# Performance work log

Measured on AMD Instinct MI355X. Metric: run time of the kernel, lower is better.

Reference implementation:

```python
import jax, jax.numpy as jnp
import numpy as np

B, S, E, H = 2, 2048, 2048, 16
D = E // H          # head_dim = 128
RD = 128            # rotary_emb_dim (== head_dim here)
BASE = 10000.0


def setup_inputs() -> dict:
    key = jax.random.key(0)
    k1, k2, k3, k4, k5 = jax.random.split(key, 5)
    scale = 0.02
    return {
        "x": jax.random.normal(k1, (B, S, E), dtype=jnp.float32),
        "wqkv_w": jax.random.normal(k2, (3 * E, E), dtype=jnp.float32) * scale,
        "wqkv_b": jax.random.normal(k3, (3 * E,), dtype=jnp.float32) * scale,
        "out_w": jax.random.normal(k4, (E, E), dtype=jnp.float32) * scale,
        "out_b": jax.random.normal(k5, (E,), dtype=jnp.float32) * scale,
    }


def _rope_cos_sin(seqlen, dtype):
    inv_freq = 1.0 / (BASE ** (jnp.arange(0, RD, 2, dtype=jnp.float32) / RD))
    t = jnp.arange(seqlen, dtype=jnp.float32)
    freqs = jnp.outer(t, inv_freq)          # (S, RD//2)
    return jnp.cos(freqs).astype(dtype), jnp.sin(freqs).astype(dtype)


def _apply_rotary(v, cos, sin):
    # v: (B, S, H, D); rotate first RD dims (here RD == D)
    v_rot, v_pass = v[..., :RD], v[..., RD:]
    v1, v2 = jnp.split(v_rot, 2, axis=-1)    # each (B, S, H, RD//2)
    c = cos[None, :, None, :]
    s = sin[None, :, None, :]
    rot = jnp.concatenate([v1 * c - v2 * s, v1 * s + v2 * c], axis=-1)
    return jnp.concatenate([rot, v_pass], axis=-1)


def reference(x, wqkv_w, wqkv_b, out_w, out_b):
    b, s, e = x.shape
    # column-parallel QKV projection (world size 1)
    qkv = jnp.einsum("bse,fe->bsf", x, wqkv_w) + wqkv_b     # (B, S, 3E)
    qkv = qkv.reshape(b, s, 3, H, D)
    cos, sin = _rope_cos_sin(s, x.dtype)
    q = _apply_rotary(qkv[:, :, 0], cos, sin)               # (B, S, H, D)
    k = _apply_rotary(qkv[:, :, 1], cos, sin)
    v = qkv[:, :, 2]
    # causal self-attention, softmax_scale = 1/sqrt(head_dim)
    scale = 1.0 / jnp.sqrt(jnp.asarray(D, dtype=x.dtype))
    scores = jnp.einsum("bshd,bthd->bhst", q, k) * scale    # (B, H, S, S)
    causal_mask = jnp.tril(jnp.ones((s, s), dtype=bool))
    scores = jnp.where(causal_mask[None, None], scores, jnp.finfo(x.dtype).min)
    probs = jax.nn.softmax(scores, axis=-1)
    ctx = jnp.einsum("bhst,bthd->bshd", probs, v)           # (B, S, H, D)
    # row-parallel output projection
    out = jnp.einsum("bse,fe->bsf", ctx.reshape(b, s, e), out_w) + out_b
    return out
```

## Files before the change

kernel.cpp:

```cpp
#include <hip/hip_runtime.h>
#include <cstdint>
#include <cstddef>

#define Bd 2
#define Sd 2048
#define Ed 2048
#define Hd 16
#define Dd 128
#define N3E 6144
#define ATT_SCALE 0.08838834764831845f

typedef short bf16x8 __attribute__((ext_vector_type(8)));
typedef float f32x4 __attribute__((ext_vector_type(4)));
typedef float f32x16 __attribute__((ext_vector_type(16)));

__device__ __forceinline__ float bf2f(unsigned short u) {
    union { unsigned int u; float f; } c;
    c.u = ((unsigned int)u) << 16;
    return c.f;
}
__device__ __forceinline__ unsigned short f2bf(float f) {
    union { float f; unsigned int u; } c;
    c.f = f;
    unsigned int x = c.u;
    x += 0x7FFFu + ((x >> 16) & 1u);
    return (unsigned short)(x >> 16);
}

__device__ __forceinline__ void gl2lds16(const void* g, void* l) {
    __builtin_amdgcn_global_load_lds(
        (const __attribute__((address_space(1))) void*)g,
        (__attribute__((address_space(3))) void*)l, 16, 0, 0);
}

__global__ void cvt_all(const float* __restrict__ x,
                        const float* __restrict__ w1,
                        const float* __restrict__ w2,
                        unsigned short* __restrict__ ox,
                        unsigned short* __restrict__ o1,
                        unsigned short* __restrict__ o2) {
    int i = (blockIdx.x * 256 + threadIdx.x) * 4;
    const float* s;
    unsigned short* d;
    int off;
    if (i < 8388608) { s = x; d = ox; off = i; }
    else if (i < 20971520) { s = w1; d = o1; off = i - 8388608; }
    else { s = w2; d = o2; off = i - 20971520; }
    const float4 v = *(const float4*)(s + off);
    d[off + 0] = f2bf(v.x);
    d[off + 1] = f2bf(v.y);
    d[off + 2] = f2bf(v.z);
    d[off + 3] = f2bf(v.w);
}

template <int MODE>
__global__ void gemm_bt(const unsigned short* __restrict__ A,
                        const unsigned short* __restrict__ Bm,
                        const float* __restrict__ bias,
                        void* __restrict__ o0, void* __restrict__ o1,
                        void* __restrict__ o2, int Ndim, int K) {
    __shared__ __align__(16) unsigned short U[16640];
    unsigned short* As = U;
    unsigned short* Bs = U + 8192;

    const int tid = threadIdx.x;
    const int lane = tid & 63;
    const int wave = tid >> 6;
    const int quad = lane >> 4;
    const int l16 = lane & 15;
    const int wr = wave >> 1;
    const int wc = wave & 1;

    const int n0 = blockIdx.x * 128;
    const int m0 = blockIdx.y * 128;

    const unsigned short* Ab = A + (size_t)m0 * K;
    const unsigned short* Bb = Bm + (size_t)n0 * K;

    const f32x4 fzero = {0.f, 0.f, 0.f, 0.f};
    f32x4 acc[4][4];
#pragma unroll
    for (int i = 0; i < 4; i++)
#pragma unroll
        for (int j = 0; j < 4; j++) acc[i][j] = fzero;

    for (int k0 = 0; k0 < K; k0 += 64) {
        __syncthreads();
#pragma unroll
        for (int it = 0; it < 4; ++it) {
            int L = it * 256 + tid;
            int row = L >> 3;
            int cs = L & 7;
            int gc = cs ^ (row & 7);
            gl2lds16(Ab + row * K + k0 + gc * 8, (void*)(As + L * 8));
            gl2lds16(Bb + row * K + k0 + gc * 8, (void*)(Bs + L * 8));
        }
        __syncthreads();
#pragma unroll
        for (int kk = 0; kk < 2; ++kk) {
            bf16x8 af[4], bfr[4];
#pragma unroll
            for (int i = 0; i < 4; i++) {
                int row = wr * 64 + i * 16 + l16;
                int cs = kk * 4 + quad;
                af[i] = *(const bf16x8*)(As + row * 64 + (cs ^ (row & 7)) * 8);
            }
#pragma unroll
            for (int j = 0; j < 4; j++) {
                int row = wc * 64 + j * 16 + l16;
                int cs = kk * 4 + quad;
                bfr[j] = *(const bf16x8*)(Bs + row * 64 + (cs ^ (row & 7)) * 8);
            }
#pragma unroll
            for (int i = 0; i < 4; i++)
#pragma unroll
                for (int j = 0; j < 4; j++)
                    acc[i][j] = __builtin_amdgcn_mfma_f32_16x16x32_bf16(
                        af[i], bfr[j], acc[i][j], 0, 0, 0);
        }
    }

    if (MODE == 0) {
#pragma unroll
        for (int j = 0; j < 4; j++) {
            int col = n0 + wc * 64 + j * 16 + l16;
            float bv = bias[col];
#pragma unroll
            for (int i = 0; i < 4; i++) {
                int rbase = m0 + wr * 64 + i * 16 + quad * 4;
#pragma unroll
                for (int r = 0; r < 4; r++)
                    ((float*)o0)[(size_t)(rbase + r) * Ndim + col] =
                        acc[i][j][r] + bv;
            }
        }
    } else {
        __syncthreads();
#pragma unroll
        for (int j = 0; j < 4; j++) {
            int coll = wc * 64 + j * 16 + l16;
            float bv = bias[n0 + coll];
#pragma unroll
            for (int i = 0; i < 4; i++) {
                int rl = wr * 64 + i * 16 + quad * 4;
#pragma unroll
                for (int r = 0; r < 4; r++)
                    U[(rl + r) * 130 + coll] = f2bf(acc[i][j][r] + bv);
            }
        }
        __syncthreads();

        const int ch = n0 >> 7;
        const int c = ch >> 4;
        const int h = ch & 15;
        const int bb = m0 >> 11;
        const int s0 = m0 & 2047;

        if (c < 2) {
            unsigned short* dstq = (unsigned short*)(c == 0 ? o0 : o1);
            const size_t hb = ((size_t)(bb * Hd + h)) * Sd;
#pragma unroll
            for (int it = 0; it < 16; ++it) {
                int lin = it * 256 + tid;
                int row = lin >> 5, p = lin & 31;
                int s = s0 + row;
                unsigned int lo = *(const unsigned int*)(U + row * 130 + 2 * p);
                unsigned int hi =
                    *(const unsigned int*)(U + row * 130 + 64 + 2 * p);
                float v1a = bf2f((unsigned short)lo), v1b = bf2f(lo >> 16);
                float v2a = bf2f((unsigned short)hi), v2b = bf2f(hi >> 16);
                float fa = (float)s * __expf(-(float)(2 * p) *
                                             (9.210340371976184f / 64.0f));
                float fb = (float)s * __expf(-(float)(2 * p + 1) *
                                             (9.210340371976184f / 64.0f));
                float sna, csa, snb, csb;
                __sincosf(fa, &sna, &csa);
                __sincosf(fb, &snb, &csb);
                ushort2 r1, r2;
                r1.x = f2bf(v1a * csa - v2a * sna);
                r1.y = f2bf(v1b * csb - v2b * snb);
                r2.x = f2bf(v1a * sna + v2a * csa);
                r2.y = f2bf(v1b * snb + v2b * csb);
                unsigned short* dst = dstq + (hb + s) * Dd;
                *(ushort2*)(dst + 2 * p) = r1;
                *(ushort2*)(dst + 64 + 2 * p) = r2;
            }
        } else {
            unsigned short* dstv = (unsigned short*)o2;
            const size_t hb = ((size_t)(bb * Hd + h)) * Dd;
#pragma unroll
            for (int it = 0; it < 16; ++it) {
                int lin = it * 256 + tid;
                int d = lin >> 5, sc = lin & 31;
                int s4 = sc * 4;
                ushort4 pk;
                pk.x = U[(s4 + 0) * 130 + d];
                pk.y = U[(s4 + 1) * 130 + d];
                pk.z = U[(s4 + 2) * 130 + d];
                pk.w = U[(s4 + 3) * 130 + d];
                *(ushort4*)(dstv + (hb + d) * Sd + s0 + s4) = pk;
            }
        }
    }
}

__global__ __launch_bounds__(256, 2) void flash_attn(
    const unsigned short* __restrict__ q, const unsigned short* __restrict__ k,
    const unsigned short* __restrict__ vt, unsigned short* __restrict__ ctx) {
    __shared__ __align__(16) unsigned short Ks[64 * 128];
    __shared__ __align__(16) unsigned short Vts[128 * 64];
    __shared__ __align__(16) unsigned short Ps[128 * 64];

    const int tid = threadIdx.x;
    const int lane = tid & 63;
    const int wave = tid >> 6;
    const int l32 = lane & 31;
    const int half = lane >> 5;

    const int yy = blockIdx.y;
    const int qi = (yy < 8) ? 15 - yy : yy - 8;
    const int bh = blockIdx.x;
    const int q0 = qi * 128;
    const int qg = q0 + wave * 32 + l32;
    const int prow = wave * 32 + l32;
    const int psw = prow & 7;

    const unsigned short* kb = k + (size_t)bh * Sd * Dd;
    const unsigned short* vtb = vt + (size_t)bh * Dd * Sd;

    bf16x8 aq[8];
    {
        const unsigned short* qrow = q + ((size_t)bh * Sd + qg) * Dd;
#pragma unroll
        for (int ks = 0; ks < 8; ks++)
            aq[ks] = *(const bf16x8*)(qrow + ks * 16 + half * 8);
    }

    f32x16 o[4];
#pragma unroll
    for (int db = 0; db < 4; db++)
#pragma unroll
        for (int r = 0; r < 16; r++) o[db][r] = 0.f;
    float mi = -3.0e38f, li = 0.f;

    const int tmax = q0 + 64;
    for (int t0 = 0; t0 <= tmax; t0 += 64) {
#pragma unroll
        for (int it = 0; it < 4; ++it) {
            int L = it * 256 + tid;
            int rk = L >> 4;
            int ck = L & 15;
            int gk = ck ^ (rk & 15);
            gl2lds16(kb + (size_t)(t0 + rk) * Dd + gk * 8, (void*)(Ks + L * 8));
            int rv = L >> 3;
            int cv = L & 7;
            int gv = cv ^ (rv & 7);
            gl2lds16(vtb + (size_t)rv * Sd + t0 + gv * 8, (void*)(Vts + L * 8));
        }
        __syncthreads();

        f32x16 sa[2];
#pragma unroll
        for (int b2 = 0; b2 < 2; b2++)
#pragma unroll
            for (int r = 0; r < 16; r++) sa[b2][r] = 0.f;
#pragma unroll
        for (int ks = 0; ks < 8; ks++) {
            int cd = ks * 2 + half;
#pragma unroll
            for (int b2 = 0; b2 < 2; b2++) {
                int row = b2 * 32 + l32;
                bf16x8 ak = *(const bf16x8*)(Ks + row * 128 +
                                             (cd ^ (row & 15)) * 8);
                sa[b2] = __builtin_amdgcn_mfma_f32_32x32x16_bf16(ak, aq[ks],
                                                                 sa[b2], 0, 0, 0);
            }
        }

        float mx = -3.0e38f;
#pragma unroll
        for (int b2 = 0; b2 < 2; b2++)
#pragma unroll
            for (int r = 0; r < 16; r++) {
                float v = sa[b2][r] * ATT_SCALE;
                int tg = t0 + b2 * 32 + (r & 3) + 8 * (r >> 2) + 4 * half;
                if (tg > qg) v = -3.0e38f;
                sa[b2][r] = v;
                mx = fmaxf(mx, v);
            }
        mx = fmaxf(mx, __shfl_xor(mx, 32, 64));
        const float mnew = fmaxf(mi, mx);
        const float alpha = __expf(mi - mnew);
        float rs = 0.f;
#pragma unroll
        for (int b2 = 0; b2 < 2; b2++)
#pragma unroll
            for (int r = 0; r < 16; r++) {
                float pp = __expf(sa[b2][r] - mnew);
                sa[b2][r] = pp;
                rs += pp;
            }
        rs += __shfl_xor(rs, 32, 64);
        li = li * alpha + rs;
        mi = mnew;

#pragma unroll
        for (int db = 0; db < 4; db++)
#pragma unroll
            for (int r = 0; r < 16; r++) o[db][r] *= alpha;

#pragma unroll
        for (int b2 = 0; b2 < 2; b2++)
#pragma unroll
            for (int g = 0; g < 4; g++) {
                ushort4 pk;
                pk.x = f2bf(sa[b2][g * 4 + 0]);
                pk.y = f2bf(sa[b2][g * 4 + 1]);
                pk.z = f2bf(sa[b2][g * 4 + 2]);
                pk.w = f2bf(sa[b2][g * 4 + 3]);
                *(ushort4*)(Ps + prow * 64 + ((b2 * 4 + g) ^ psw) * 8 +
                            half * 4) = pk;
            }
        __syncthreads();

#pragma unroll
        for (int kk = 0; kk < 4; kk++) {
            bf16x8 bp = *(const bf16x8*)(Ps + prow * 64 +
                                         ((kk * 2 + half) ^ psw) * 8);
#pragma unroll
            for (int db = 0; db < 4; db++) {
                int row = db * 32 + l32;
                bf16x8 av = *(const bf16x8*)(
                    Vts + row * 64 + ((kk * 2 + half) ^ (row & 7)) * 8);
                o[db] = __builtin_amdgcn_mfma_f32_32x32x16_bf16(av, bp, o[db],
                                                                0, 0, 0);
            }
        }
        __syncthreads();
    }

    const int b = bh >> 4;
    const int h = bh & 15;
    const float inv = 1.0f / li;
    unsigned short* dst = ctx + ((size_t)(b * Sd + qg)) * Ed + h * Dd;
#pragma unroll
    for (int db = 0; db < 4; db++)
#pragma unroll
        for (int g = 0; g < 4; g++) {
            ushort4 pk;
            pk.x = f2bf(o[db][g * 4 + 0] * inv);
            pk.y = f2bf(o[db][g * 4 + 1] * inv);
            pk.z = f2bf(o[db][g * 4 + 2] * inv);
            pk.w = f2bf(o[db][g * 4 + 3] * inv);
            *(ushort4*)(dst + db * 32 + g * 8 + half * 4) = pk;
        }
}

extern "C" void kernel_launch(void* const* d_in, const int* in_sizes, int n_in,
                              void* d_out, int out_size, void* d_ws,
                              size_t ws_size, hipStream_t stream) {
    const float* x = (const float*)d_in[0];
    const float* wqkv_w = (const float*)d_in[1];
    const float* wqkv_b = (const float*)d_in[2];
    const float* out_w = (const float*)d_in[3];
    const float* out_b = (const float*)d_in[4];
    float* out = (float*)d_out;

    char* ws = (char*)d_ws;
    unsigned short* xb    = (unsigned short*)(ws + 0);
    unsigned short* wqkvb = (unsigned short*)(ws + 16777216);
    unsigned short* owb   = (unsigned short*)(ws + 41943040);
    unsigned short* qb    = (unsigned short*)(ws + 50331648);
    unsigned short* kb    = (unsigned short*)(ws + 67108864);
    unsigned short* vtb   = (unsigned short*)(ws + 83886080);
    unsigned short* ctx   = (unsigned short*)(ws + 0);

    cvt_all<<<24576, 256, 0, stream>>>(x, wqkv_w, out_w, xb, wqkvb, owb);
    gemm_bt<1><<<dim3(48, 32), 256, 0, stream>>>(xb, wqkvb, wqkv_b, qb, kb, vtb,
                                                 N3E, Ed);
    flash_attn<<<dim3(32, 16), 256, 0, stream>>>(qb, kb, vtb, ctx);
    gemm_bt<0><<<dim3(16, 32), 256, 0, stream>>>(ctx, owb, out_b, out, nullptr,
                                                 nullptr, Ed, Ed);
}
```

Baseline: 348.5 us.

## Triple-buffer GEMM LDS tiles with 256x128 blocks and split-phase MFMA scheduling

Each GEMM block now computes a 256x128 tile with 512 threads instead of 128x128 with 256. The K loop uses a three-slot LDS ring that prefetches two k-tiles ahead with direct global-to-LDS loads, tracked by explicit vmcnt waits. Each k-step is split into two halves that interleave prefetch issue, fragment loads and MFMA bursts, with s_setprio raised around the MFMAs. The goal is to hide global load latency and halve B-tile reloads per output, at the cost of about 147KB of LDS per block, which limits each CU to one block.

```diff
diff --git a/kernel.cpp b/kernel.cpp
--- a/kernel.cpp
+++ b/kernel.cpp
@@ -54,14 +54,14 @@
 }
 
 template <int MODE>
-__global__ void gemm_bt(const unsigned short* __restrict__ A,
-                        const unsigned short* __restrict__ Bm,
-                        const float* __restrict__ bias,
-                        void* __restrict__ o0, void* __restrict__ o1,
-                        void* __restrict__ o2, int Ndim, int K) {
-    __shared__ __align__(16) unsigned short U[16640];
-    unsigned short* As = U;
-    unsigned short* Bs = U + 8192;
+__global__ __launch_bounds__(512, 2) void gemm_bt(
+    const unsigned short* __restrict__ A,
+    const unsigned short* __restrict__ Bm,
+    const float* __restrict__ bias,
+    void* __restrict__ o0, void* __restrict__ o1,
+    void* __restrict__ o2, int Ndim, int K) {
+    __shared__ __align__(16) unsigned short As[3 * 256 * 64];
+    __shared__ __align__(16) unsigned short Bs[3 * 128 * 64];
 
     const int tid = threadIdx.x;
     const int lane = tid & 63;
@@ -72,10 +72,10 @@
     const int wc = wave & 1;
 
     const int n0 = blockIdx.x * 128;
-    const int m0 = blockIdx.y * 128;
-
+    const int m0 = blockIdx.y * 256;
     const unsigned short* Ab = A + (size_t)m0 * K;
     const unsigned short* Bb = Bm + (size_t)n0 * K;
+    const int NT = K >> 6;
 
     const f32x4 fzero = {0.f, 0.f, 0.f, 0.f};
     f32x4 acc[4][4];
@@ -84,40 +84,94 @@
 #pragma unroll
         for (int j = 0; j < 4; j++) acc[i][j] = fzero;
 
-    for (int k0 = 0; k0 < K; k0 += 64) {
-        __syncthreads();
-#pragma unroll
-        for (int it = 0; it < 4; ++it) {
-            int L = it * 256 + tid;
+    auto stA = [&](int slot, int k0, int half) {
+#pragma unroll
+        for (int it = 0; it < 2; ++it) {
+            int L = (half * 2 + it) * 512 + tid;
             int row = L >> 3;
             int cs = L & 7;
             int gc = cs ^ (row & 7);
-            gl2lds16(Ab + row * K + k0 + gc * 8, (void*)(As + L * 8));
-            gl2lds16(Bb + row * K + k0 + gc * 8, (void*)(Bs + L * 8));
-        }
-        __syncthreads();
-#pragma unroll
-        for (int kk = 0; kk < 2; ++kk) {
-            bf16x8 af[4], bfr[4];
-#pragma unroll
-            for (int i = 0; i < 4; i++) {
-                int row = wr * 64 + i * 16 + l16;
-                int cs = kk * 4 + quad;
-                af[i] = *(const bf16x8*)(As + row * 64 + (cs ^ (row & 7)) * 8);
-            }
-#pragma unroll
-            for (int j = 0; j < 4; j++) {
-                int row = wc * 64 + j * 16 + l16;
-                int cs = kk * 4 + quad;
-                bfr[j] = *(const bf16x8*)(Bs + row * 64 + (cs ^ (row & 7)) * 8);
-            }
-#pragma unroll
-            for (int i = 0; i < 4; i++)
+            gl2lds16(Ab + (size_t)row * K + k0 + gc * 8,
+                     (void*)(As + slot * 16384 + L * 8));
+        }
+    };
+    auto stB = [&](int slot, int k0, int half) {
+        int L = half * 512 + tid;
+        int row = L >> 3;
+        int cs = L & 7;
+        int gc = cs ^ (row & 7);
+        gl2lds16(Bb + (size_t)row * K + k0 + gc * 8,
+                 (void*)(Bs + slot * 8192 + L * 8));
+    };
+
+    stA(0, 0, 0); stB(0, 0, 0); stA(0, 0, 1); stB(0, 0, 1);
+    stA(1, 64, 0); stB(1, 64, 0); stA(1, 64, 1); stB(1, 64, 1);
+    asm volatile("s_waitcnt vmcnt(6)" ::: "memory");
+    __builtin_amdgcn_s_barrier();
+
+    for (int t = 0; t < NT; ++t) {
+        const int sc = t % 3;
+        const int sp = (t + 2) % 3;
+        const int k2 = (t + 2) << 6;
+        const unsigned short* Asl = As + sc * 16384;
+        const unsigned short* Bsl = Bs + sc * 8192;
+        const bool pf = (t + 2 < NT);
+
+        if (pf) { stA(sp, k2, 0); stB(sp, k2, 0); }
+        bf16x8 bfr[4][2], af0[2][2];
+#pragma unroll
+        for (int j = 0; j < 4; j++) {
+            int row = wc * 64 + j * 16 + l16;
+#pragma unroll
+            for (int kk = 0; kk < 2; kk++)
+                bfr[j][kk] = *(const bf16x8*)(
+                    Bsl + row * 64 + (((kk * 4 + quad) ^ (row & 7))) * 8);
+        }
+#pragma unroll
+        for (int i = 0; i < 2; i++) {
+            int row = wr * 64 + i * 16 + l16;
+#pragma unroll
+            for (int kk = 0; kk < 2; kk++)
+                af0[i][kk] = *(const bf16x8*)(
+                    Asl + row * 64 + (((kk * 4 + quad) ^ (row & 7))) * 8);
+        }
+        __builtin_amdgcn_s_barrier();
+        __builtin_amdgcn_s_setprio(1);
+#pragma unroll
+        for (int kk = 0; kk < 2; kk++)
+#pragma unroll
+            for (int i = 0; i < 2; i++)
 #pragma unroll
                 for (int j = 0; j < 4; j++)
                     acc[i][j] = __builtin_amdgcn_mfma_f32_16x16x32_bf16(
-                        af[i], bfr[j], acc[i][j], 0, 0, 0);
-        }
+                        af0[i][kk], bfr[j][kk], acc[i][j], 0, 0, 0);
+        __builtin_amdgcn_s_setprio(0);
+        __builtin_amdgcn_s_barrier();
+
+        if (pf) { stA(sp, k2, 1); stB(sp, k2, 1); }
+        bf16x8 af1[2][2];
+#pragma unroll
+        for (int i = 0; i < 2; i++) {
+            int row = wr * 64 + (i + 2) * 16 + l16;
+#pragma unroll
+            for (int kk = 0; kk < 2; kk++)
+                af1[i][kk] = *(const bf16x8*)(
+                    Asl + row * 64 + (((kk * 4 + quad) ^ (row & 7))) * 8);
+        }
+        __builtin_amdgcn_s_barrier();
+        __builtin_amdgcn_s_setprio(1);
+#pragma unroll
+        for (int kk = 0; kk < 2; kk++)
+#pragma unroll
+            for (int i = 0; i < 2; i++)
+#pragma unroll
+                for (int j = 0; j < 4; j++)
+                    acc[i + 2][j] = __builtin_amdgcn_mfma_f32_16x16x32_bf16(
+                        af1[i][kk], bfr[j][kk], acc[i + 2][j], 0, 0, 0);
+        __builtin_amdgcn_s_setprio(0);
+        if (pf) asm volatile("s_waitcnt vmcnt(6)" ::: "memory");
+        else    asm volatile("s_waitcnt vmcnt(0)" ::: "memory");
+        __builtin_amdgcn_s_barrier();
     }
 
     if (MODE == 0) {
@@ -135,7 +189,7 @@
             }
         }
     } else {
-        __syncthreads();
+        unsigned short* U = As;
 #pragma unroll
         for (int j = 0; j < 4; j++) {
             int coll = wc * 64 + j * 16 + l16;
@@ -161,7 +215,7 @@
             const size_t hb = ((size_t)(bb * Hd + h)) * Sd;
 #pragma unroll
             for (int it = 0; it < 16; ++it) {
-                int lin = it * 256 + tid;
+                int lin = it * 512 + tid;
                 int row = lin >> 5, p = lin & 31;
                 int s = s0 + row;
                 unsigned int lo = *(const unsigned int*)(U + row * 130 + 2 * p);
@@ -190,9 +244,9 @@
             const size_t hb = ((size_t)(bb * Hd + h)) * Dd;
 #pragma unroll
             for (int it = 0; it < 16; ++it) {
-                int lin = it * 256 + tid;
-                int d = lin >> 5, sc = lin & 31;
-                int s4 = sc * 4;
+                int lin = it * 512 + tid;
+                int d = lin >> 6, sc2 = lin & 63;
+                int s4 = sc2 * 4;
                 ushort4 pk;
                 pk.x = U[(s4 + 0) * 130 + d];
                 pk.y = U[(s4 + 1) * 130 + d];
@@ -376,9 +430,9 @@
     unsigned short* ctx   = (unsigned short*)(ws + 0);
 
     cvt_all<<<24576, 256, 0, stream>>>(x, wqkv_w, out_w, xb, wqkvb, owb);
-    gemm_bt<1><<<dim3(48, 32), 256, 0, stream>>>(xb, wqkvb, wqkv_b, qb, kb, vtb,
+    gemm_bt<1><<<dim3(48, 16), 512, 0, stream>>>(xb, wqkvb, wqkv_b, qb, kb, vtb,
                                                  N3E, Ed);
     flash_attn<<<dim3(32, 16), 256, 0, stream>>>(qb, kb, vtb, ctx);
-    gemm_bt<0><<<dim3(16, 32), 256, 0, stream>>>(ctx, owb, out_b, out, nullptr,
+    gemm_bt<0><<<dim3(16, 16), 512, 0, stream>>>(ctx, owb, out_b, out, nullptr,
                                                  nullptr, Ed, Ed);
 }
```

New measurement: 450.2 us. 1.29x slower.
